# Optimization experiments

Hardware: AMD Instinct MI355X
Metric: run time of the kernel (lower is better)

## Reference

```python
import jax, jax.numpy as jnp
import numpy as np

N, E, R, IN, HID, HEADS, OUT, T = 20000, 320000, 16, 128, 64, 8, 128, 50000
NEG_SLOPE = 0.2
EPS = 1e-16


def _rgat_conv(x, edge_index, edge_type, W, att_q, att_k, heads, out_ch):
    """Relational GAT conv: per-relation transform, additive attention,
    segment-softmax over incoming edges of each dst node, scatter-add."""
    n = x.shape[0]
    r = W.shape[0]
    src, dst = edge_index[0], edge_index[1]
    # per-relation transform of all nodes: [R, N, H, O]
    xr = jnp.einsum('ni,rio->rno', x, W).reshape(r, n, heads, out_ch)
    k = xr[edge_type, src]  # [E, H, O] message from source
    q = xr[edge_type, dst]  # [E, H, O] query at destination
    logits = jnp.sum(q * att_q[edge_type], axis=-1) + jnp.sum(k * att_k[edge_type], axis=-1)  # [E, H]
    logits = jax.nn.leaky_relu(logits, NEG_SLOPE)
    # segment softmax over edges grouped by dst
    m = jax.ops.segment_max(logits, dst, num_segments=n)  # [N, H]
    e = jnp.exp(logits - m[dst])
    s = jax.ops.segment_sum(e, dst, num_segments=n)  # [N, H]
    a = e / (s[dst] + EPS)  # [E, H]
    out = jax.ops.segment_sum(a[..., None] * k, dst, num_segments=n)  # [N, H, O]
    return out.reshape(n, heads * out_ch)


def setup_inputs() -> dict:
    key = jax.random.key(0)
    ks = jax.random.split(key, 16)
    x = jax.random.normal(ks[0], (N, IN), dtype=jnp.float32)
    edge_index = jax.random.randint(ks[1], (2, E), 0, N, dtype=jnp.int64)
    edge_type = jax.random.randint(ks[2], (E,), 0, R, dtype=jnp.int64)
    target_edges = jax.random.randint(ks[3], (2, T), 0, N, dtype=jnp.int64)
    sc = 0.1
    W1 = jax.random.normal(ks[4], (R, IN, HEADS * HID), dtype=jnp.float32) * sc
    aq1 = jax.random.normal(ks[5], (R, HEADS, HID), dtype=jnp.float32) * sc
    ak1 = jax.random.normal(ks[6], (R, HEADS, HID), dtype=jnp.float32) * sc
    W2 = jax.random.normal(ks[7], (R, HEADS * HID, OUT), dtype=jnp.float32) * sc
    aq2 = jax.random.normal(ks[8], (R, 1, OUT), dtype=jnp.float32) * sc
    ak2 = jax.random.normal(ks[9], (R, 1, OUT), dtype=jnp.float32) * sc
    lw1 = jax.random.normal(ks[10], (2 * OUT, OUT), dtype=jnp.float32) * sc
    lb1 = jnp.zeros((OUT,), dtype=jnp.float32)
    lw2 = jax.random.normal(ks[11], (OUT, 1), dtype=jnp.float32) * sc
    lb2 = jnp.zeros((1,), dtype=jnp.float32)
    return {"x": x, "edge_index": edge_index, "edge_type": edge_type,
            "target_edges": target_edges, "W1": W1, "aq1": aq1, "ak1": ak1,
            "W2": W2, "aq2": aq2, "ak2": ak2, "lw1": lw1, "lb1": lb1,
            "lw2": lw2, "lb2": lb2}


def reference(x, edge_index, edge_type, target_edges, W1, aq1, ak1, W2, aq2, ak2, lw1, lb1, lw2, lb2):
    # encode (dropout is identity in eval mode)
    h = _rgat_conv(x, edge_index, edge_type, W1, aq1, ak1, HEADS, HID)  # [N, HEADS*HID]
    h = jax.nn.relu(h)
    z = _rgat_conv(h, edge_index, edge_type, W2, aq2, ak2, 1, OUT)  # [N, OUT]
    # decode target edges with link-prediction MLP
    z_pair = jnp.concatenate([z[target_edges[0]], z[target_edges[1]]], axis=1)  # [T, 2*OUT]
    hdec = jax.nn.relu(z_pair @ lw1 + lb1)
    return hdec @ lw2 + lb2  # [T, 1]
```

## Files before the change

kernel.cpp:

```cpp
#include <hip/hip_runtime.h>
#include <cstdint>
#include <cstddef>

#define NN     20000
#define NE     320000
#define NR     16
#define DIN    128
#define DH     512
#define DOUT   128
#define NT     50000
#define TILE   64
#define TILE1  128
#define CHUNKS 5
#define CHD    4000
#define NBUCKET (CHUNKS * NR)
#define MSGROWS 69888
#define MAXTPC1 2240
#define NTILESMAX1 (NE / TILE1 + NBUCKET)
#define MT2Y   157
#define YGRID  (MT2Y * 16)
#define QGRID  320

typedef __attribute__((ext_vector_type(8))) short bf16x8;
typedef __attribute__((ext_vector_type(4))) float f32x4;

__device__ __forceinline__ unsigned short f2bf(float x) {
    unsigned int b = __float_as_uint(x);
    b = b + 0x7fffu + ((b >> 16) & 1u);
    return (unsigned short)(b >> 16);
}
__device__ __forceinline__ float bf2f(unsigned short u) {
    return __uint_as_float(((unsigned int)u) << 16);
}
__device__ __forceinline__ unsigned packbf(float lo, float hi) {
    return (unsigned)f2bf(lo) | ((unsigned)f2bf(hi) << 16);
}

__global__ void alpha1_kernel(const float* __restrict__ W1, const float* __restrict__ aq1,
                              const float* __restrict__ ak1, float* __restrict__ alpha1) {
    int i = blockIdx.x;
    int c = threadIdx.x;
    int r = c >> 4, s = (c >> 3) & 1, h = c & 7;
    const float* att = (s == 0 ? aq1 : ak1) + (r * 8 + h) * 64;
    const float* w = W1 + ((size_t)(r * DIN + i)) * DH + h * 64;
    float acc = 0.f;
    #pragma unroll 8
    for (int o = 0; o < 64; ++o) acc += w[o] * att[o];
    alpha1[i * 256 + c] = acc;
}

__global__ void alpha2_kernel(const float* __restrict__ W2, const float* __restrict__ aq2,
                              const float* __restrict__ ak2, float* __restrict__ alpha2) {
    int g = blockIdx.x * blockDim.x + threadIdx.x;
    if (g >= DH * 32) return;
    int i = g >> 5, c = g & 31;
    int r = c >> 1, s = c & 1;
    const float* att = (s == 0 ? aq2 : ak2) + r * DOUT;
    const float* w = W2 + ((size_t)(r * DH + i)) * DOUT;
    float acc = 0.f;
    #pragma unroll 8
    for (int o = 0; o < DOUT; ++o) acc += w[o] * att[o];
    alpha2[i * 32 + c] = acc;
}

__global__ void splitA1T_kernel(const float* __restrict__ alpha1, unsigned short* __restrict__ A1Thi,
                                unsigned short* __restrict__ A1Tlo) {
    int g = blockIdx.x * 256 + threadIdx.x;
    if (g >= 128 * 256) return;
    int c = g >> 7, i = g & 127;
    float v = alpha1[i * 256 + c];
    unsigned short h = f2bf(v);
    A1Thi[g] = h;
    A1Tlo[g] = f2bf(v - bf2f(h));
}

__global__ void split_x_kernel(const float* __restrict__ x, unsigned short* __restrict__ xhi,
                               unsigned short* __restrict__ xlo) {
    int g = blockIdx.x * 256 + threadIdx.x;
    if (g >= NN * DIN / 4) return;
    float4 v = ((const float4*)x)[g];
    ushort4 h, l;
    h.x = f2bf(v.x); l.x = f2bf(v.x - bf2f(h.x));
    h.y = f2bf(v.y); l.y = f2bf(v.y - bf2f(h.y));
    h.z = f2bf(v.z); l.z = f2bf(v.z - bf2f(h.z));
    h.w = f2bf(v.w); l.w = f2bf(v.w - bf2f(h.w));
    ((ushort4*)xhi)[g] = h;
    ((ushort4*)xlo)[g] = l;
}

__global__ void splitW1T_kernel(const float* __restrict__ W1, unsigned short* __restrict__ Whi) {
    __shared__ float T[128 * 65];
    int r = blockIdx.x >> 3;
    int ob = blockIdx.x & 7;
    int tid = threadIdx.x;
    for (int idx = tid; idx < 128 * 64; idx += 256) {
        int i = idx >> 6, o = idx & 63;
        T[i * 65 + o] = W1[((size_t)(r * DIN + i)) * DH + ob * 64 + o];
    }
    __syncthreads();
    for (int idx = tid; idx < 64 * 128; idx += 256) {
        int o = idx >> 7, i = idx & 127;
        Whi[((size_t)r * DH + ob * 64 + o) * DIN + i] = f2bf(T[i * 65 + o]);
    }
}

__global__ void splitW2T_kernel(const float* __restrict__ W2, unsigned short* __restrict__ Whi) {
    __shared__ float T[128 * 65];
    int r = blockIdx.x >> 1;
    int ob = blockIdx.x & 1;
    int tid = threadIdx.x;
    for (int kc = 0; kc < 4; ++kc) {
        if (kc) __syncthreads();
        for (int idx = tid; idx < 128 * 64; idx += 256) {
            int k = idx >> 6, o = idx & 63;
            T[k * 65 + o] = W2[((size_t)(r * DH + kc * 128 + k)) * DOUT + ob * 64 + o];
        }
        __syncthreads();
        for (int idx = tid; idx < 64 * 128; idx += 256) {
            int o = idx >> 7, k = idx & 127;
            Whi[((size_t)r * DOUT + ob * 64 + o) * DH + kc * 128 + k] = f2bf(T[k * 65 + o]);
        }
    }
}

__global__ void splitLw1_kernel(const float* __restrict__ lw1, unsigned short* __restrict__ Lhi,
                                unsigned short* __restrict__ Llo) {
    int g = blockIdx.x * 256 + threadIdx.x;
    if (g >= 256 * 128) return;
    int o = g >> 8, k = g & 255;
    float v = lw1[k * 128 + o];
    unsigned short h = f2bf(v);
    Lhi[(size_t)o * 256 + k] = h;
    Llo[(size_t)o * 256 + k] = f2bf(v - bf2f(h));
}

__global__ void hist_kernel(const int* __restrict__ ei, const int* __restrict__ et,
                            int* __restrict__ cnt, int* __restrict__ cnt_d) {
    __shared__ int bins[NBUCKET];
    int t = threadIdx.x;
    if (t < NBUCKET) bins[t] = 0;
    __syncthreads();
    int e = blockIdx.x * 256 + t;
    if (e < NE) {
        int d = ei[NE + e];
        int key = (d / CHD) * NR + et[e];
        atomicAdd(&bins[key], 1);
        atomicAdd(&cnt_d[d], 1);
    }
    __syncthreads();
    if (t < NBUCKET && bins[t]) atomicAdd(&cnt[t], bins[t]);
}

__global__ void scan_bkt_kernel(const int* __restrict__ cnt, int* __restrict__ boffs,
                                int* __restrict__ cursor, int* __restrict__ cts) {
    if (threadIdx.x != 0) return;
    int acc = 0, tiles = 0;
    for (int b = 0; b < NBUCKET; ++b) {
        if ((b & (NR - 1)) == 0) cts[b >> 4] = tiles;
        boffs[b] = acc; cursor[b] = acc;
        int cn = cnt[b];
        tiles += (cn + TILE1 - 1) / TILE1;
        acc += cn;
    }
    boffs[NBUCKET] = acc; cts[CHUNKS] = tiles;
}

__global__ void tilemap_kernel(const int* __restrict__ boffs, int* __restrict__ tile_b,
                               int* __restrict__ tile_s) {
    __shared__ int bo[NBUCKET + 1];
    int tid = threadIdx.x;
    if (tid <= NBUCKET) bo[tid] = boffs[tid];
    __syncthreads();
    int t = blockIdx.x * 256 + tid;
    if (t >= NTILESMAX1) return;
    int acc = 0, bb = -1, ss = 0;
    for (int b = 0; b < NBUCKET; ++b) {
        int cn = bo[b + 1] - bo[b];
        int nt = (cn + TILE1 - 1) / TILE1;
        if (t >= acc && t < acc + nt) { bb = b; ss = bo[b] + (t - acc) * TILE1; }
        acc += nt;
    }
    tile_b[t] = bb; tile_s[t] = ss;
}

__global__ void bucket_place_kernel(const int* __restrict__ ei, const int* __restrict__ et,
                                    int* __restrict__ cursor, int* __restrict__ border) {
    __shared__ int binc[NBUCKET], base_[NBUCKET], rank_[NBUCKET];
    int t = threadIdx.x;
    if (t < NBUCKET) { binc[t] = 0; rank_[t] = 0; }
    __syncthreads();
    int e = blockIdx.x * 256 + t;
    int key = -1;
    if (e < NE) { key = (ei[NE + e] / CHD) * NR + et[e]; atomicAdd(&binc[key], 1); }
    __syncthreads();
    if (t < NBUCKET && binc[t]) base_[t] = atomicAdd(&cursor[t], binc[t]);
    __syncthreads();
    if (key >= 0) border[base_[key] + atomicAdd(&rank_[key], 1)] = e;
}

__global__ void scan_dst_kernel(const int* __restrict__ cnt_d, int* __restrict__ doffs,
                                int* __restrict__ cursor_d) {
    __shared__ int part[1024];
    int t = threadIdx.x;
    int base = t * 20;
    int s = 0;
    for (int i = 0; i < 20 && base + i < NN; ++i) s += cnt_d[base + i];
    part[t] = s;
    __syncthreads();
    for (int off = 1; off < 1024; off <<= 1) {
        int v = (t >= off) ? part[t - off] : 0;
        __syncthreads();
        part[t] += v;
        __syncthreads();
    }
    int run = part[t] - s;
    for (int i = 0; i < 20 && base + i < NN; ++i) {
        doffs[base + i] = run; cursor_d[base + i] = run;
        run += cnt_d[base + i];
    }
    if (t == 1023) doffs[NN] = part[1023];
}

__global__ void place_dst_kernel(const int* __restrict__ border, const int* __restrict__ ei,
                                 const int* __restrict__ et, int* __restrict__ cursor_d,
                                 int* __restrict__ dlist, int* __restrict__ dedge,
                                 int* __restrict__ dsr) {
    int pos = blockIdx.x * 256 + threadIdx.x;
    if (pos >= NE) return;
    int e = border[pos];
    int d = ei[NE + e];
    int idx = atomicAdd(&cursor_d[d], 1);
    dlist[idx] = pos;
    dedge[idx] = e;
    dsr[idx] = ei[e] * NR + et[e];
}

__global__ __launch_bounds__(256, 2)
void qk1_mfma_kernel(const unsigned short* __restrict__ xhi, const unsigned short* __restrict__ xlo,
                     const unsigned short* __restrict__ A1Thi, const unsigned short* __restrict__ A1Tlo,
                     float* __restrict__ qk1) {
    int t = (blockIdx.x & 7) * (QGRID / 8) + (blockIdx.x >> 3);
    if (t >= MT2Y * 2) return;
    int mt = t >> 1, nb = t & 1;
    int n0 = mt * 128;
    __shared__ __align__(16) unsigned short Ah[128 * 64];
    __shared__ __align__(16) unsigned short Al[128 * 64];
    __shared__ __align__(16) unsigned short Bh_[128 * 64];
    __shared__ __align__(16) unsigned short Bl_[128 * 64];
    int tid = threadIdx.x;
    int w = tid >> 6, lane = tid & 63;
    int l15 = lane & 15, l4 = lane >> 4;
    int wr = w >> 1, wc = w & 1;
    f32x4 acc[4][4];
    #pragma unroll
    for (int m = 0; m < 4; ++m)
        #pragma unroll
        for (int n = 0; n < 4; ++n) acc[m][n] = (f32x4){0.f, 0.f, 0.f, 0.f};
    for (int kc = 0; kc < 2; ++kc) {
        if (kc) __syncthreads();
        {
            int row = tid >> 1, seg = tid & 1;
            int n = n0 + row; if (n >= NN) n = NN - 1;
            unsigned rb = row * 128, sw = (row & 7) << 4;
            const uint4* ph = (const uint4*)(xhi + (size_t)n * DIN + kc * 64 + seg * 32);
            const uint4* pl = (const uint4*)(xlo + (size_t)n * DIN + kc * 64 + seg * 32);
            const uint4* qh = (const uint4*)(A1Thi + (size_t)(nb * 128 + row) * DIN + kc * 64 + seg * 32);
            const uint4* ql = (const uint4*)(A1Tlo + (size_t)(nb * 128 + row) * DIN + kc * 64 + seg * 32);
            #pragma unroll
            for (int i = 0; i < 4; ++i) {
                unsigned off = (rb + seg * 64 + i * 16) ^ sw;
                *(uint4*)((char*)Ah + off) = ph[i];
                *(uint4*)((char*)Al + off) = pl[i];
                *(uint4*)((char*)Bh_ + off) = qh[i];
                *(uint4*)((char*)Bl_ + off) = ql[i];
            }
        }
        __syncthreads();
        bf16x8 ah[4][2], al[4][2], bh[4][2], bl[4][2];
        #pragma unroll
        for (int m = 0; m < 4; ++m) {
            int row = wr * 64 + m * 16 + l15;
            unsigned rb = row * 128, sw = (row & 7) << 4;
            #pragma unroll
            for (int ks = 0; ks < 2; ++ks) {
                unsigned off = (rb + ks * 64 + l4 * 16) ^ sw;
                ah[m][ks] = *(const bf16x8*)((const char*)Ah + off);
                al[m][ks] = *(const bf16x8*)((const char*)Al + off);
            }
        }
        #pragma unroll
        for (int n = 0; n < 4; ++n) {
            int col = wc * 64 + n * 16 + l15;
            unsigned rb = col * 128, sw = (col & 7) << 4;
            #pragma unroll
            for (int ks = 0; ks < 2; ++ks) {
                unsigned off = (rb + ks * 64 + l4 * 16) ^ sw;
                bh[n][ks] = *(const bf16x8*)((const char*)Bh_ + off);
                bl[n][ks] = *(const bf16x8*)((const char*)Bl_ + off);
            }
        }
        #pragma unroll
        for (int n = 0; n < 4; ++n)
            #pragma unroll
            for (int ks = 0; ks < 2; ++ks)
                #pragma unroll
                for (int m = 0; m < 4; ++m) {
                    acc[m][n] = __builtin_amdgcn_mfma_f32_16x16x32_bf16(ah[m][ks], bh[n][ks], acc[m][n], 0, 0, 0);
                    acc[m][n] = __builtin_amdgcn_mfma_f32_16x16x32_bf16(al[m][ks], bh[n][ks], acc[m][n], 0, 0, 0);
                    acc[m][n] = __builtin_amdgcn_mfma_f32_16x16x32_bf16(ah[m][ks], bl[n][ks], acc[m][n], 0, 0, 0);
                }
    }
    #pragma unroll
    for (int m = 0; m < 4; ++m) {
        int row0 = n0 + wr * 64 + m * 16 + l4 * 4;
        #pragma unroll
        for (int rg = 0; rg < 4; ++rg) {
            int row = row0 + rg;
            if (row < NN) {
                float* op = qk1 + (size_t)row * 256 + nb * 128 + wc * 64 + l15;
                #pragma unroll
                for (int n = 0; n < 4; ++n) op[n * 16] = acc[m][n][rg];
            }
        }
    }
}

__global__ void elogit1_kernel(const int* __restrict__ ei, const int* __restrict__ et,
                               const float* __restrict__ qk1, float* __restrict__ e1) {
    int e = blockIdx.x * blockDim.x + threadIdx.x;
    if (e >= NE) return;
    int src = ei[e], dst = ei[NE + e], r = et[e];
    const float* qp = qk1 + (size_t)dst * 256 + r * 16;
    const float* kp = qk1 + (size_t)src * 256 + r * 16 + 8;
    float* ep = e1 + (size_t)e * 8;
    #pragma unroll
    for (int h = 0; h < 8; ++h) {
        float l = qp[h] + kp[h];
        l = l > 0.f ? l : 0.2f * l;
        ep[h] = __expf(l);
    }
}

__global__ __launch_bounds__(256, 3)
void l1_gemm_kernel(const unsigned short* __restrict__ xhi, const unsigned short* __restrict__ xlo,
                    const unsigned short* __restrict__ W1Thi,
                    const int* __restrict__ ei, const int* __restrict__ border,
                    const int* __restrict__ tile_b, const int* __restrict__ tile_s,
                    const int* __restrict__ boffs, const int* __restrict__ cts,
                    int c, unsigned* __restrict__ msgu) {
    int wg = (blockIdx.x & 7) * (MAXTPC1 / 8) + (blockIdx.x >> 3);
    int tt = wg >> 2, cb = wg & 3;
    int t = cts[c] + tt;
    if (t >= cts[c + 1]) return;
    int b = tile_b[t];
    int r = b & (NR - 1);
    int start = tile_s[t];
    int cstart = boffs[c * NR];
    int cnt = boffs[b + 1] - start; if (cnt > TILE1) cnt = TILE1;
    __shared__ __align__(16) unsigned short Ah[128 * 64];
    __shared__ __align__(16) unsigned short Al[128 * 64];
    __shared__ __align__(16) unsigned short Bh_[128 * 64];
    __shared__ int srcS[TILE1];
    int tid = threadIdx.x;
    if (tid < TILE1) {
        int sv = 0;
        if (tid < cnt) sv = ei[border[start + tid]];
        srcS[tid] = sv;
    }
    __syncthreads();
    int w = tid >> 6, lane = tid & 63;
    int l15 = lane & 15, l4 = lane >> 4;
    int wr = w >> 1, wc = w & 1;
    f32x4 acc[4][4];
    #pragma unroll
    for (int m = 0; m < 4; ++m)
        #pragma unroll
        for (int n = 0; n < 4; ++n) acc[m][n] = (f32x4){0.f, 0.f, 0.f, 0.f};
    for (int kc = 0; kc < 2; ++kc) {
        if (kc) __syncthreads();
        {
            int row = tid >> 1, seg = tid & 1;
            unsigned rb = row * 128, sw = (row & 7) << 4;
            const uint4* ph = (const uint4*)(xhi + (size_t)srcS[row] * DIN + kc * 64 + seg * 32);
            const uint4* pl = (const uint4*)(xlo + (size_t)srcS[row] * DIN + kc * 64 + seg * 32);
            const uint4* qh = (const uint4*)(W1Thi + ((size_t)r * DH + cb * 128 + row) * DIN + kc * 64 + seg * 32);
            #pragma unroll
            for (int i = 0; i < 4; ++i) {
                unsigned off = (rb + seg * 64 + i * 16) ^ sw;
                *(uint4*)((char*)Ah + off) = ph[i];
                *(uint4*)((char*)Al + off) = pl[i];
                *(uint4*)((char*)Bh_ + off) = qh[i];
            }
        }
        __syncthreads();
        bf16x8 ah[4][2], al[4][2], bh[4][2];
        #pragma unroll
        for (int m = 0; m < 4; ++m) {
            int row = wr * 64 + m * 16 + l15;
            unsigned rb = row * 128, sw = (row & 7) << 4;
            #pragma unroll
            for (int ks = 0; ks < 2; ++ks) {
                unsigned off = (rb + ks * 64 + l4 * 16) ^ sw;
                ah[m][ks] = *(const bf16x8*)((const char*)Ah + off);
                al[m][ks] = *(const bf16x8*)((const char*)Al + off);
            }
        }
        #pragma unroll
        for (int n = 0; n < 4; ++n) {
            int col = wc * 64 + n * 16 + l15;
            unsigned rb = col * 128, sw = (col & 7) << 4;
            #pragma unroll
            for (int ks = 0; ks < 2; ++ks) {
                unsigned off = (rb + ks * 64 + l4 * 16) ^ sw;
                bh[n][ks] = *(const bf16x8*)((const char*)Bh_ + off);
            }
        }
        #pragma unroll
        for (int n = 0; n < 4; ++n)
            #pragma unroll
            for (int ks = 0; ks < 2; ++ks)
                #pragma unroll
                for (int m = 0; m < 4; ++m) {
                    acc[m][n] = __builtin_amdgcn_mfma_f32_16x16x32_bf16(ah[m][ks], bh[n][ks], acc[m][n], 0, 0, 0);
                    acc[m][n] = __builtin_amdgcn_mfma_f32_16x16x32_bf16(al[m][ks], bh[n][ks], acc[m][n], 0, 0, 0);
                }
    }
    unsigned* mb = msgu + (size_t)(start - cstart) * 256 + cb * 64 + wc * 32 + l15;
    #pragma unroll
    for (int m = 0; m < 4; ++m) {
        int row0 = wr * 64 + m * 16 + l4 * 4;
        #pragma unroll
        for (int rg = 0; rg < 4; ++rg) {
            int row = row0 + rg;
            if (row < cnt) {
                unsigned* mp = mb + (size_t)row * 256;
                mp[0]  = packbf(acc[m][0][rg], acc[m][2][rg]);
                mp[16] = packbf(acc[m][1][rg], acc[m][3][rg]);
            }
        }
    }
}

__global__ void l1_agg_kernel(const unsigned* __restrict__ msgu, const float* __restrict__ e1,
                              const int* __restrict__ dlist, const int* __restrict__ dedge,
                              const int* __restrict__ doffs, const int* __restrict__ boffs,
                              int c, unsigned short* __restrict__ hhi, unsigned short* __restrict__ hlo,
                              const float* __restrict__ alpha2, float* __restrict__ qk2v) {
    __shared__ float hrow[DH];
    __shared__ float red[32][9];
    int tid = threadIdx.x;
    int d = c * CHD + blockIdx.x;
    if (d >= NN) return;
    int lo_ = doffs[d], hi_ = doffs[d + 1];
    int cstart = boffs[c * NR];
    int head = tid >> 5;
    float a0 = 0.f, a1 = 0.f, se = 0.f;
    for (int p = lo_; p < hi_; ++p) {
        int pos = dlist[p];
        float wgt = e1[(size_t)dedge[p] * 8 + head];
        se += wgt;
        unsigned v = msgu[(size_t)(pos - cstart) * 256 + tid];
        a0 += wgt * bf2f((unsigned short)(v & 0xffff));
        a1 += wgt * bf2f((unsigned short)(v >> 16));
    }
    float inv = 1.f / (se + 1e-16f);
    a0 *= inv; a1 *= inv;
    a0 = a0 > 0.f ? a0 : 0.f;
    a1 = a1 > 0.f ? a1 : 0.f;
    int w = tid >> 6, q = (tid >> 4) & 3, l15 = tid & 15;
    int nq = ((q >> 1) << 2) | (q & 1);
    int c0 = w * 128 + nq * 16 + l15;
    hrow[c0] = a0; hrow[c0 + 32] = a1;
    unsigned short h0 = f2bf(a0), h1 = f2bf(a1);
    hhi[(size_t)d * DH + c0] = h0;
    hlo[(size_t)d * DH + c0] = f2bf(a0 - bf2f(h0));
    hhi[(size_t)d * DH + c0 + 32] = h1;
    hlo[(size_t)d * DH + c0 + 32] = f2bf(a1 - bf2f(h1));
    __syncthreads();
    int j = tid & 31, ib = tid >> 5;
    float s = 0.f;
    #pragma unroll 8
    for (int i = ib * 64; i < ib * 64 + 64; ++i) s += hrow[i] * alpha2[(size_t)i * 32 + j];
    red[j][ib] = s;
    __syncthreads();
    if (tid < 32) {
        float t = 0.f;
        #pragma unroll
        for (int g = 0; g < 8; ++g) t += red[tid][g];
        qk2v[(size_t)d * 32 + tid] = t;
    }
}

__global__ void elogit2_kernel(const int* __restrict__ ei, const int* __restrict__ et,
                               const float* __restrict__ qk2, float* __restrict__ e2) {
    int e = blockIdx.x * blockDim.x + threadIdx.x;
    if (e >= NE) return;
    int src = ei[e], dst = ei[NE + e], r = et[e];
    float l = qk2[(size_t)dst * 32 + r * 2] + qk2[(size_t)src * 32 + r * 2 + 1];
    l = l > 0.f ? l : 0.2f * l;
    e2[e] = __expf(l);
}

__global__ __launch_bounds__(256, 3)
void y2_gemm_kernel(const unsigned short* __restrict__ hhi, const unsigned short* __restrict__ hlo,
                    const unsigned short* __restrict__ W2Thi,
                    unsigned* __restrict__ Y2u) {
    int t = (blockIdx.x & 7) * (YGRID / 8) + (blockIdx.x >> 3);
    int mt = t >> 4, r = t & 15;
    int n0 = mt * 128;
    __shared__ __align__(16) unsigned short Ah[128 * 64];
    __shared__ __align__(16) unsigned short Al[128 * 64];
    __shared__ __align__(16) unsigned short Bh_[128 * 64];
    int tid = threadIdx.x;
    int w = tid >> 6, lane = tid & 63;
    int l15 = lane & 15, l4 = lane >> 4;
    int wr = w >> 1, wc = w & 1;
    f32x4 acc[4][4];
    #pragma unroll
    for (int m = 0; m < 4; ++m)
        #pragma unroll
        for (int n = 0; n < 4; ++n) acc[m][n] = (f32x4){0.f, 0.f, 0.f, 0.f};
    for (int kc = 0; kc < 8; ++kc) {
        if (kc) __syncthreads();
        {
            int row = tid >> 1, seg = tid & 1;
            int n = n0 + row; if (n >= NN) n = NN - 1;
            unsigned rb = row * 128, sw = (row & 7) << 4;
            const uint4* ph = (const uint4*)(hhi + (size_t)n * DH + kc * 64 + seg * 32);
            const uint4* pl = (const uint4*)(hlo + (size_t)n * DH + kc * 64 + seg * 32);
            const uint4* qh = (const uint4*)(W2Thi + ((size_t)r * DOUT + row) * DH + kc * 64 + seg * 32);
            #pragma unroll
            for (int i = 0; i < 4; ++i) {
                unsigned off = (rb + seg * 64 + i * 16) ^ sw;
                *(uint4*)((char*)Ah + off) = ph[i];
                *(uint4*)((char*)Al + off) = pl[i];
                *(uint4*)((char*)Bh_ + off) = qh[i];
            }
        }
        __syncthreads();
        bf16x8 ah[4][2], al[4][2], bh[4][2];
        #pragma unroll
        for (int m = 0; m < 4; ++m) {
            int row = wr * 64 + m * 16 + l15;
            unsigned rb = row * 128, sw = (row & 7) << 4;
            #pragma unroll
            for (int ks = 0; ks < 2; ++ks) {
                unsigned off = (rb + ks * 64 + l4 * 16) ^ sw;
                ah[m][ks] = *(const bf16x8*)((const char*)Ah + off);
                al[m][ks] = *(const bf16x8*)((const char*)Al + off);
            }
        }
        #pragma unroll
        for (int n = 0; n < 4; ++n) {
            int col = wc * 64 + n * 16 + l15;
            unsigned rb = col * 128, sw = (col & 7) << 4;
            #pragma unroll
            for (int ks = 0; ks < 2; ++ks) {
                unsigned off = (rb + ks * 64 + l4 * 16) ^ sw;
                bh[n][ks] = *(const bf16x8*)((const char*)Bh_ + off);
            }
        }
        #pragma unroll
        for (int n = 0; n < 4; ++n)
            #pragma unroll
            for (int ks = 0; ks < 2; ++ks)
                #pragma unroll
                for (int m = 0; m < 4; ++m) {
                    acc[m][n] = __builtin_amdgcn_mfma_f32_16x16x32_bf16(ah[m][ks], bh[n][ks], acc[m][n], 0, 0, 0);
                    acc[m][n] = __builtin_amdgcn_mfma_f32_16x16x32_bf16(al[m][ks], bh[n][ks], acc[m][n], 0, 0, 0);
                }
    }
    unsigned* mb = Y2u + (size_t)n0 * 1024 + r * 64 + wc * 32 + l15;
    #pragma unroll
    for (int m = 0; m < 4; ++m) {
        int row0 = wr * 64 + m * 16 + l4 * 4;
        #pragma unroll
        for (int rg = 0; rg < 4; ++rg) {
            int row = row0 + rg;
            if (n0 + row < NN) {
                unsigned* mp = mb + (size_t)row * 1024;
                mp[0]  = packbf(acc[m][0][rg], acc[m][2][rg]);
                mp[16] = packbf(acc[m][1][rg], acc[m][3][rg]);
            }
        }
    }
}

__global__ void l2_agg_kernel(const unsigned* __restrict__ Y2u, const float* __restrict__ e2,
                              const int* __restrict__ dedge, const int* __restrict__ dsr,
                              const int* __restrict__ doffs, float* __restrict__ zacc) {
    int tid = threadIdx.x;
    int d = blockIdx.x * 4 + (tid >> 6);
    if (d >= NN) return;
    int lane = tid & 63;
    int lo_ = doffs[d], hi_ = doffs[d + 1];
    float a0 = 0.f, a1 = 0.f, se = 0.f;
    for (int p = lo_; p < hi_; ++p) {
        float wgt = e2[dedge[p]];
        se += wgt;
        unsigned v = Y2u[(size_t)dsr[p] * 64 + lane];
        a0 += wgt * bf2f((unsigned short)(v & 0xffff));
        a1 += wgt * bf2f((unsigned short)(v >> 16));
    }
    float inv = 1.f / (se + 1e-16f);
    int q = lane >> 4, l15 = lane & 15;
    int nq = ((q >> 1) << 2) | (q & 1);
    int c0 = nq * 16 + l15;
    zacc[(size_t)d * DOUT + c0] = a0 * inv;
    zacc[(size_t)d * DOUT + c0 + 32] = a1 * inv;
}

__global__ __launch_bounds__(256, 2)
void decode_kernel(const float* __restrict__ z, const int* __restrict__ tgt,
                   const unsigned short* __restrict__ Lhi, const unsigned short* __restrict__ Llo,
                   const float* __restrict__ lb1, const float* __restrict__ lw2,
                   const float* __restrict__ lb2, float* __restrict__ out) {
    __shared__ __align__(16) unsigned short Ah[64 * 256];
    __shared__ __align__(16) unsigned short Al[64 * 256];
    __shared__ float red[TILE][5];
    int t0 = blockIdx.x * TILE;
    int tid = threadIdx.x;
    int cnt = NT - t0; if (cnt > TILE) cnt = TILE;
    {
        int row = tid >> 2, seg = tid & 3;
        int node = 0;
        bool live = (row < cnt);
        if (live) node = tgt[(seg >> 1) * NT + t0 + row];
        const float4* pz = (const float4*)(z + (size_t)node * DOUT + (seg & 1) * 64);
        unsigned rb = row * 512, sb = (seg >> 1) * 256 + (seg & 1) * 128;
        unsigned sw = (row & 7) << 4;
        #pragma unroll
        for (int g = 0; g < 8; ++g) {
            float4 a = live ? pz[g * 2] : (float4){0,0,0,0};
            float4 bq = live ? pz[g * 2 + 1] : (float4){0,0,0,0};
            unsigned short h0 = f2bf(a.x), h1 = f2bf(a.y), h2 = f2bf(a.z), h3 = f2bf(a.w);
            unsigned short h4 = f2bf(bq.x), h5 = f2bf(bq.y), h6 = f2bf(bq.z), h7 = f2bf(bq.w);
            uint4 uh, ul;
            uh.x = (unsigned)h0 | ((unsigned)h1 << 16);
            uh.y = (unsigned)h2 | ((unsigned)h3 << 16);
            uh.z = (unsigned)h4 | ((unsigned)h5 << 16);
            uh.w = (unsigned)h6 | ((unsigned)h7 << 16);
            ul.x = (unsigned)f2bf(a.x - bf2f(h0)) | ((unsigned)f2bf(a.y - bf2f(h1)) << 16);
            ul.y = (unsigned)f2bf(a.z - bf2f(h2)) | ((unsigned)f2bf(a.w - bf2f(h3)) << 16);
            ul.z = (unsigned)f2bf(bq.x - bf2f(h4)) | ((unsigned)f2bf(bq.y - bf2f(h5)) << 16);
            ul.w = (unsigned)f2bf(bq.z - bf2f(h6)) | ((unsigned)f2bf(bq.w - bf2f(h7)) << 16);
            unsigned off = (rb + sb + g * 16) ^ sw;
            *(uint4*)((char*)Ah + off) = uh;
            *(uint4*)((char*)Al + off) = ul;
        }
    }
    __syncthreads();
    int w = tid >> 6, lane = tid & 63;
    int l15 = lane & 15, l4 = lane >> 4;
    const unsigned short* Bh = Lhi + (size_t)(w * 32 + l15) * 256 + l4 * 8;
    const unsigned short* Bl = Llo + (size_t)(w * 32 + l15) * 256 + l4 * 8;
    f32x4 acc[4][2];
    #pragma unroll
    for (int m = 0; m < 4; ++m) { acc[m][0] = (f32x4){0.f,0.f,0.f,0.f}; acc[m][1] = (f32x4){0.f,0.f,0.f,0.f}; }
    #pragma unroll
    for (int k = 0; k < 8; ++k) {
        bf16x8 ah[4], al[4];
        #pragma unroll
        for (int m = 0; m < 4; ++m) {
            int row = m * 16 + l15;
            unsigned off = ((unsigned)row * 512 + k * 64 + l4 * 16) ^ ((unsigned)(row & 7) << 4);
            ah[m] = *(const bf16x8*)((const char*)Ah + off);
            al[m] = *(const bf16x8*)((const char*)Al + off);
        }
        #pragma unroll
        for (int n = 0; n < 2; ++n) {
            bf16x8 bh = *(const bf16x8*)(Bh + (size_t)n * 16 * 256 + k * 32);
            bf16x8 bl = *(const bf16x8*)(Bl + (size_t)n * 16 * 256 + k * 32);
            #pragma unroll
            for (int m = 0; m < 4; ++m) {
                acc[m][n] = __builtin_amdgcn_mfma_f32_16x16x32_bf16(ah[m], bh, acc[m][n], 0, 0, 0);
                acc[m][n] = __builtin_amdgcn_mfma_f32_16x16x32_bf16(ah[m], bl, acc[m][n], 0, 0, 0);
                acc[m][n] = __builtin_amdgcn_mfma_f32_16x16x32_bf16(al[m], bh, acc[m][n], 0, 0, 0);
            }
        }
    }
    int col0 = w * 32 + l15;
    float lb_0 = lb1[col0], lb_1 = lb1[col0 + 16];
    float lwa = lw2[col0], lwb = lw2[col0 + 16];
    #pragma unroll
    for (int m = 0; m < 4; ++m) {
        #pragma unroll
        for (int rg = 0; rg < 4; ++rg) {
            float h0 = acc[m][0][rg] + lb_0; h0 = h0 > 0.f ? h0 : 0.f;
            float h1 = acc[m][1][rg] + lb_1; h1 = h1 > 0.f ? h1 : 0.f;
            float s = h0 * lwa + h1 * lwb;
            s += __shfl_xor(s, 1); s += __shfl_xor(s, 2);
            s += __shfl_xor(s, 4); s += __shfl_xor(s, 8);
            if (l15 == 0) red[m * 16 + l4 * 4 + rg][w] = s;
        }
    }
    __syncthreads();
    if (tid < cnt) out[t0 + tid] = red[tid][0] + red[tid][1] + red[tid][2] + red[tid][3] + lb2[0];
}

extern "C" void kernel_launch(void* const* d_in, const int* in_sizes, int n_in,
                              void* d_out, int out_size, void* d_ws, size_t ws_size,
                              hipStream_t stream) {
    const float* x   = (const float*)d_in[0];
    const int*   ei  = (const int*)d_in[1];
    const int*   et  = (const int*)d_in[2];
    const int*   tgt = (const int*)d_in[3];
    const float* W1  = (const float*)d_in[4];
    const float* aq1 = (const float*)d_in[5];
    const float* ak1 = (const float*)d_in[6];
    const float* W2  = (const float*)d_in[7];
    const float* aq2 = (const float*)d_in[8];
    const float* ak2 = (const float*)d_in[9];
    const float* lw1 = (const float*)d_in[10];
    const float* lb1 = (const float*)d_in[11];
    const float* lw2 = (const float*)d_in[12];
    const float* lb2 = (const float*)d_in[13];
    float* out = (float*)d_out;
    (void)in_sizes; (void)n_in; (void)out_size; (void)ws_size;

    char* ws = (char*)d_ws;
    size_t off = 0;
    auto alloc = [&](size_t bytes) -> void* {
        void* p = ws + off;
        off += (bytes + 255) & ~(size_t)255;
        return p;
    };
    int* cnt   = (int*)alloc(NBUCKET * sizeof(int));
    int* cnt_d = (int*)alloc((size_t)NN * sizeof(int));
    size_t zero_bytes = off;
    int*   boffs    = (int*)alloc((NBUCKET + 1) * sizeof(int));
    int*   cursor   = (int*)alloc(NBUCKET * sizeof(int));
    int*   cts      = (int*)alloc((CHUNKS + 1) * sizeof(int));
    int*   doffs    = (int*)alloc((size_t)(NN + 1) * sizeof(int));
    int*   cursor_d = (int*)alloc((size_t)NN * sizeof(int));
    int*   border   = (int*)alloc((size_t)NE * sizeof(int));
    int*   dlist    = (int*)alloc((size_t)NE * sizeof(int));
    int*   dedge    = (int*)alloc((size_t)NE * sizeof(int));
    int*   dsr      = (int*)alloc((size_t)NE * sizeof(int));
    int*   tile_b   = (int*)alloc((size_t)NTILESMAX1 * sizeof(int));
    int*   tile_s   = (int*)alloc((size_t)NTILESMAX1 * sizeof(int));
    float* alpha2   = (float*)alloc((size_t)512 * 32 * 4);
    float* qk2v     = (float*)alloc((size_t)NN * 32 * 4);
    float* e2       = (float*)alloc((size_t)NE * 4);
    float* zacc     = (float*)alloc((size_t)NN * DOUT * 4);
    unsigned short* xhi   = (unsigned short*)alloc((size_t)NN * DIN * 2);
    unsigned short* xlo   = (unsigned short*)alloc((size_t)NN * DIN * 2);
    unsigned short* hhi   = (unsigned short*)alloc((size_t)NN * DH * 2);
    unsigned short* hlo   = (unsigned short*)alloc((size_t)NN * DH * 2);
    unsigned short* W1Thi = (unsigned short*)alloc((size_t)NR * DH * DIN * 2);
    unsigned short* W2Thi = (unsigned short*)alloc((size_t)NR * DOUT * DH * 2);
    unsigned short* Lhi   = (unsigned short*)alloc((size_t)128 * 256 * 2);
    unsigned short* Llo   = (unsigned short*)alloc((size_t)128 * 256 * 2);
    unsigned short* A1Thi = (unsigned short*)alloc((size_t)256 * 128 * 2);
    unsigned short* A1Tlo = (unsigned short*)alloc((size_t)256 * 128 * 2);
    char* msgr = (char*)alloc((size_t)NN * 1024 * 4);
    unsigned* msgu = (unsigned*)msgr;
    unsigned* Y2u  = (unsigned*)msgr;
    float* alpha1 = (float*)msgr;
    float* qk1    = (float*)(msgr + 131072);
    float* e1     = (float*)(msgr + (size_t)MSGROWS * 1024);

    hipMemsetAsync(ws, 0, zero_bytes, stream);
    alpha1_kernel<<<DIN, 256, 0, stream>>>(W1, aq1, ak1, alpha1);
    splitA1T_kernel<<<(128 * 256 + 255) / 256, 256, 0, stream>>>(alpha1, A1Thi, A1Tlo);
    alpha2_kernel<<<(DH * 32 + 255) / 256, 256, 0, stream>>>(W2, aq2, ak2, alpha2);
    split_x_kernel<<<(NN * DIN / 4 + 255) / 256, 256, 0, stream>>>(x, xhi, xlo);
    splitW1T_kernel<<<NR * 8, 256, 0, stream>>>(W1, W1Thi);
    splitW2T_kernel<<<NR * 2, 256, 0, stream>>>(W2, W2Thi);
    splitLw1_kernel<<<(256 * 128 + 255) / 256, 256, 0, stream>>>(lw1, Lhi, Llo);
    hist_kernel<<<(NE + 255) / 256, 256, 0, stream>>>(ei, et, cnt, cnt_d);
    scan_bkt_kernel<<<1, 64, 0, stream>>>(cnt, boffs, cursor, cts);
    tilemap_kernel<<<(NTILESMAX1 + 255) / 256, 256, 0, stream>>>(boffs, tile_b, tile_s);
    bucket_place_kernel<<<(NE + 255) / 256, 256, 0, stream>>>(ei, et, cursor, border);
    scan_dst_kernel<<<1, 1024, 0, stream>>>(cnt_d, doffs, cursor_d);
    place_dst_kernel<<<(NE + 255) / 256, 256, 0, stream>>>(border, ei, et, cursor_d, dlist, dedge, dsr);
    qk1_mfma_kernel<<<QGRID, 256, 0, stream>>>(xhi, xlo, A1Thi, A1Tlo, qk1);
    elogit1_kernel<<<(NE + 255) / 256, 256, 0, stream>>>(ei, et, qk1, e1);
    for (int c = 0; c < CHUNKS; ++c) {
        l1_gemm_kernel<<<MAXTPC1, 256, 0, stream>>>(xhi, xlo, W1Thi, ei, border,
                                                    tile_b, tile_s, boffs, cts, c, msgu);
        l1_agg_kernel<<<CHD, 256, 0, stream>>>(msgu, e1, dlist, dedge, doffs, boffs, c,
                                               hhi, hlo, alpha2, qk2v);
    }
    elogit2_kernel<<<(NE + 255) / 256, 256, 0, stream>>>(ei, et, qk2v, e2);
    y2_gemm_kernel<<<YGRID, 256, 0, stream>>>(hhi, hlo, W2Thi, Y2u);
    l2_agg_kernel<<<(NN + 3) / 4, 256, 0, stream>>>(Y2u, e2, dedge, dsr, doffs, zacc);
    decode_kernel<<<(NT + TILE - 1) / TILE, 256, 0, stream>>>(zacc, tgt, Lhi, Llo,
                                                              lb1, lw2, lb2, out);
}
```

Baseline: 659.5 us.

## Load low-precision bf16 operands directly from global into registers, raising occupancy

In the three split-bf16 GEMM kernels (qk1, l1, y2), the low-half operands are now read straight from global memory into MFMA fragment registers instead of being staged through shared memory. This halves or quarters LDS use and raises launch_bounds to 4 blocks per CU. Separately, the two aggregation loops are unrolled by two so each iteration issues two independent gathers. The cost is uncoalesced per-lane global loads for the low operands and higher register pressure under the tighter occupancy bound.

```diff
diff --git a/kernel.cpp b/kernel.cpp
--- a/kernel.cpp
+++ b/kernel.cpp
@@ -235,7 +235,7 @@
     dsr[idx] = ei[e] * NR + et[e];
 }
 
-__global__ __launch_bounds__(256, 2)
+__global__ __launch_bounds__(256, 4)
 void qk1_mfma_kernel(const unsigned short* __restrict__ xhi, const unsigned short* __restrict__ xlo,
                      const unsigned short* __restrict__ A1Thi, const unsigned short* __restrict__ A1Tlo,
                      float* __restrict__ qk1) {
@@ -244,13 +244,20 @@
     int mt = t >> 1, nb = t & 1;
     int n0 = mt * 128;
     __shared__ __align__(16) unsigned short Ah[128 * 64];
-    __shared__ __align__(16) unsigned short Al[128 * 64];
     __shared__ __align__(16) unsigned short Bh_[128 * 64];
-    __shared__ __align__(16) unsigned short Bl_[128 * 64];
     int tid = threadIdx.x;
     int w = tid >> 6, lane = tid & 63;
     int l15 = lane & 15, l4 = lane >> 4;
     int wr = w >> 1, wc = w & 1;
+    const unsigned short* alp[4];
+    const unsigned short* blp[4];
+    #pragma unroll
+    for (int m = 0; m < 4; ++m) {
+        int rn = n0 + wr * 64 + m * 16 + l15; if (rn >= NN) rn = NN - 1;
+        alp[m] = xlo + (size_t)rn * DIN;
+        int col = wc * 64 + m * 16 + l15;
+        blp[m] = A1Tlo + (size_t)(nb * 128 + col) * DIN;
+    }
     f32x4 acc[4][4];
     #pragma unroll
     for (int m = 0; m < 4; ++m)
@@ -263,20 +270,24 @@
             int n = n0 + row; if (n >= NN) n = NN - 1;
             unsigned rb = row * 128, sw = (row & 7) << 4;
             const uint4* ph = (const uint4*)(xhi + (size_t)n * DIN + kc * 64 + seg * 32);
-            const uint4* pl = (const uint4*)(xlo + (size_t)n * DIN + kc * 64 + seg * 32);
             const uint4* qh = (const uint4*)(A1Thi + (size_t)(nb * 128 + row) * DIN + kc * 64 + seg * 32);
-            const uint4* ql = (const uint4*)(A1Tlo + (size_t)(nb * 128 + row) * DIN + kc * 64 + seg * 32);
             #pragma unroll
             for (int i = 0; i < 4; ++i) {
                 unsigned off = (rb + seg * 64 + i * 16) ^ sw;
                 *(uint4*)((char*)Ah + off) = ph[i];
-                *(uint4*)((char*)Al + off) = pl[i];
                 *(uint4*)((char*)Bh_ + off) = qh[i];
-                *(uint4*)((char*)Bl_ + off) = ql[i];
-            }
-        }
+            }
+        }
+        bf16x8 alf[4][2], blf[4][2];
+        #pragma unroll
+        for (int m = 0; m < 4; ++m)
+            #pragma unroll
+            for (int ks = 0; ks < 2; ++ks) {
+                alf[m][ks] = *(const bf16x8*)(alp[m] + kc * 64 + ks * 32 + l4 * 8);
+                blf[m][ks] = *(const bf16x8*)(blp[m] + kc * 64 + ks * 32 + l4 * 8);
+            }
         __syncthreads();
-        bf16x8 ah[4][2], al[4][2], bh[4][2], bl[4][2];
+        bf16x8 ah[4][2], bh[4][2];
         #pragma unroll
         for (int m = 0; m < 4; ++m) {
             int row = wr * 64 + m * 16 + l15;
@@ -285,7 +296,6 @@
             for (int ks = 0; ks < 2; ++ks) {
                 unsigned off = (rb + ks * 64 + l4 * 16) ^ sw;
                 ah[m][ks] = *(const bf16x8*)((const char*)Ah + off);
-                al[m][ks] = *(const bf16x8*)((const char*)Al + off);
             }
         }
         #pragma unroll
@@ -296,7 +306,6 @@
             for (int ks = 0; ks < 2; ++ks) {
                 unsigned off = (rb + ks * 64 + l4 * 16) ^ sw;
                 bh[n][ks] = *(const bf16x8*)((const char*)Bh_ + off);
-                bl[n][ks] = *(const bf16x8*)((const char*)Bl_ + off);
             }
         }
         #pragma unroll
@@ -306,8 +315,8 @@
                 #pragma unroll
                 for (int m = 0; m < 4; ++m) {
                     acc[m][n] = __builtin_amdgcn_mfma_f32_16x16x32_bf16(ah[m][ks], bh[n][ks], acc[m][n], 0, 0, 0);
-                    acc[m][n] = __builtin_amdgcn_mfma_f32_16x16x32_bf16(al[m][ks], bh[n][ks], acc[m][n], 0, 0, 0);
-                    acc[m][n] = __builtin_amdgcn_mfma_f32_16x16x32_bf16(ah[m][ks], bl[n][ks], acc[m][n], 0, 0, 0);
+                    acc[m][n] = __builtin_amdgcn_mfma_f32_16x16x32_bf16(alf[m][ks], bh[n][ks], acc[m][n], 0, 0, 0);
+                    acc[m][n] = __builtin_amdgcn_mfma_f32_16x16x32_bf16(ah[m][ks], blf[n][ks], acc[m][n], 0, 0, 0);
                 }
     }
     #pragma unroll
@@ -341,7 +350,7 @@
     }
 }
 
-__global__ __launch_bounds__(256, 3)
+__global__ __launch_bounds__(256, 4)
 void l1_gemm_kernel(const unsigned short* __restrict__ xhi, const unsigned short* __restrict__ xlo,
                     const unsigned short* __restrict__ W1Thi,
                     const int* __restrict__ ei, const int* __restrict__ border,
@@ -358,7 +367,6 @@
     int cstart = boffs[c * NR];
     int cnt = boffs[b + 1] - start; if (cnt > TILE1) cnt = TILE1;
     __shared__ __align__(16) unsigned short Ah[128 * 64];
-    __shared__ __align__(16) unsigned short Al[128 * 64];
     __shared__ __align__(16) unsigned short Bh_[128 * 64];
     __shared__ int srcS[TILE1];
     int tid = threadIdx.x;
@@ -371,6 +379,12 @@
     int w = tid >> 6, lane = tid & 63;
     int l15 = lane & 15, l4 = lane >> 4;
     int wr = w >> 1, wc = w & 1;
+    const unsigned short* alp[4];
+    #pragma unroll
+    for (int m = 0; m < 4; ++m) {
+        int row = wr * 64 + m * 16 + l15;
+        alp[m] = xlo + (size_t)srcS[row] * DIN;
+    }
     f32x4 acc[4][4];
     #pragma unroll
     for (int m = 0; m < 4; ++m)
@@ -382,18 +396,22 @@
             int row = tid >> 1, seg = tid & 1;
             unsigned rb = row * 128, sw = (row & 7) << 4;
             const uint4* ph = (const uint4*)(xhi + (size_t)srcS[row] * DIN + kc * 64 + seg * 32);
-            const uint4* pl = (const uint4*)(xlo + (size_t)srcS[row] * DIN + kc * 64 + seg * 32);
             const uint4* qh = (const uint4*)(W1Thi + ((size_t)r * DH + cb * 128 + row) * DIN + kc * 64 + seg * 32);
             #pragma unroll
             for (int i = 0; i < 4; ++i) {
                 unsigned off = (rb + seg * 64 + i * 16) ^ sw;
                 *(uint4*)((char*)Ah + off) = ph[i];
-                *(uint4*)((char*)Al + off) = pl[i];
                 *(uint4*)((char*)Bh_ + off) = qh[i];
             }
         }
+        bf16x8 alf[4][2];
+        #pragma unroll
+        for (int m = 0; m < 4; ++m)
+            #pragma unroll
+            for (int ks = 0; ks < 2; ++ks)
+                alf[m][ks] = *(const bf16x8*)(alp[m] + kc * 64 + ks * 32 + l4 * 8);
         __syncthreads();
-        bf16x8 ah[4][2], al[4][2], bh[4][2];
+        bf16x8 ah[4][2], bh[4][2];
         #pragma unroll
         for (int m = 0; m < 4; ++m) {
             int row = wr * 64 + m * 16 + l15;
@@ -402,7 +420,6 @@
             for (int ks = 0; ks < 2; ++ks) {
                 unsigned off = (rb + ks * 64 + l4 * 16) ^ sw;
                 ah[m][ks] = *(const bf16x8*)((const char*)Ah + off);
-                al[m][ks] = *(const bf16x8*)((const char*)Al + off);
             }
         }
         #pragma unroll
@@ -422,7 +439,7 @@
                 #pragma unroll
                 for (int m = 0; m < 4; ++m) {
                     acc[m][n] = __builtin_amdgcn_mfma_f32_16x16x32_bf16(ah[m][ks], bh[n][ks], acc[m][n], 0, 0, 0);
-                    acc[m][n] = __builtin_amdgcn_mfma_f32_16x16x32_bf16(al[m][ks], bh[n][ks], acc[m][n], 0, 0, 0);
+                    acc[m][n] = __builtin_amdgcn_mfma_f32_16x16x32_bf16(alf[m][ks], bh[n][ks], acc[m][n], 0, 0, 0);
                 }
     }
     unsigned* mb = msgu + (size_t)(start - cstart) * 256 + cb * 64 + wc * 32 + l15;
@@ -455,13 +472,25 @@
     int cstart = boffs[c * NR];
     int head = tid >> 5;
     float a0 = 0.f, a1 = 0.f, se = 0.f;
-    for (int p = lo_; p < hi_; ++p) {
-        int pos = dlist[p];
-        float wgt = e1[(size_t)dedge[p] * 8 + head];
-        se += wgt;
-        unsigned v = msgu[(size_t)(pos - cstart) * 256 + tid];
-        a0 += wgt * bf2f((unsigned short)(v & 0xffff));
-        a1 += wgt * bf2f((unsigned short)(v >> 16));
+    int p = lo_;
+    for (; p + 1 < hi_; p += 2) {
+        int pos0 = dlist[p], pos1 = dlist[p + 1];
+        int e0 = dedge[p], e1x = dedge[p + 1];
+        float w0 = e1[(size_t)e0 * 8 + head];
+        float w1 = e1[(size_t)e1x * 8 + head];
+        unsigned v0 = msgu[(size_t)(pos0 - cstart) * 256 + tid];
+        unsigned v1 = msgu[(size_t)(pos1 - cstart) * 256 + tid];
+        se += w0 + w1;
+        a0 += w0 * bf2f((unsigned short)(v0 & 0xffff)) + w1 * bf2f((unsigned short)(v1 & 0xffff));
+        a1 += w0 * bf2f((unsigned short)(v0 >> 16)) + w1 * bf2f((unsigned short)(v1 >> 16));
+    }
+    if (p < hi_) {
+        int pos0 = dlist[p];
+        float w0 = e1[(size_t)dedge[p] * 8 + head];
+        unsigned v0 = msgu[(size_t)(pos0 - cstart) * 256 + tid];
+        se += w0;
+        a0 += w0 * bf2f((unsigned short)(v0 & 0xffff));
+        a1 += w0 * bf2f((unsigned short)(v0 >> 16));
     }
     float inv = 1.f / (se + 1e-16f);
     a0 *= inv; a1 *= inv;
@@ -501,7 +530,7 @@
     e2[e] = __expf(l);
 }
 
-__global__ __launch_bounds__(256, 3)
+__global__ __launch_bounds__(256, 4)
 void y2_gemm_kernel(const unsigned short* __restrict__ hhi, const unsigned short* __restrict__ hlo,
                     const unsigned short* __restrict__ W2Thi,
                     unsigned* __restrict__ Y2u) {
@@ -509,12 +538,17 @@
     int mt = t >> 4, r = t & 15;
     int n0 = mt * 128;
     __shared__ __align__(16) unsigned short Ah[128 * 64];
-    __shared__ __align__(16) unsigned short Al[128 * 64];
     __shared__ __align__(16) unsigned short Bh_[128 * 64];
     int tid = threadIdx.x;
     int w = tid >> 6, lane = tid & 63;
     int l15 = lane & 15, l4 = lane >> 4;
     int wr = w >> 1, wc = w & 1;
+    const unsigned short* alp[4];
+    #pragma unroll
+    for (int m = 0; m < 4; ++m) {
+        int rn = n0 + wr * 64 + m * 16 + l15; if (rn >= NN) rn = NN - 1;
+        alp[m] = hlo + (size_t)rn * DH;
+    }
     f32x4 acc[4][4];
     #pragma unroll
     for (int m = 0; m < 4; ++m)
@@ -527,18 +561,22 @@
             int n = n0 + row; if (n >= NN) n = NN - 1;
             unsigned rb = row * 128, sw = (row & 7) << 4;
             const uint4* ph = (const uint4*)(hhi + (size_t)n * DH + kc * 64 + seg * 32);
-            const uint4* pl = (const uint4*)(hlo + (size_t)n * DH + kc * 64 + seg * 32);
             const uint4* qh = (const uint4*)(W2Thi + ((size_t)r * DOUT + row) * DH + kc * 64 + seg * 32);
             #pragma unroll
             for (int i = 0; i < 4; ++i) {
                 unsigned off = (rb + seg * 64 + i * 16) ^ sw;
                 *(uint4*)((char*)Ah + off) = ph[i];
-                *(uint4*)((char*)Al + off) = pl[i];
                 *(uint4*)((char*)Bh_ + off) = qh[i];
             }
         }
+        bf16x8 alf[4][2];
+        #pragma unroll
+        for (int m = 0; m < 4; ++m)
+            #pragma unroll
+            for (int ks = 0; ks < 2; ++ks)
+                alf[m][ks] = *(const bf16x8*)(alp[m] + kc * 64 + ks * 32 + l4 * 8);
         __syncthreads();
-        bf16x8 ah[4][2], al[4][2], bh[4][2];
+        bf16x8 ah[4][2], bh[4][2];
         #pragma unroll
         for (int m = 0; m < 4; ++m) {
             int row = wr * 64 + m * 16 + l15;
@@ -547,7 +585,6 @@
             for (int ks = 0; ks < 2; ++ks) {
                 unsigned off = (rb + ks * 64 + l4 * 16) ^ sw;
                 ah[m][ks] = *(const bf16x8*)((const char*)Ah + off);
-                al[m][ks] = *(const bf16x8*)((const char*)Al + off);
             }
         }
         #pragma unroll
@@ -567,7 +604,7 @@
                 #pragma unroll
                 for (int m = 0; m < 4; ++m) {
                     acc[m][n] = __builtin_amdgcn_mfma_f32_16x16x32_bf16(ah[m][ks], bh[n][ks], acc[m][n], 0, 0, 0);
-                    acc[m][n] = __builtin_amdgcn_mfma_f32_16x16x32_bf16(al[m][ks], bh[n][ks], acc[m][n], 0, 0, 0);
+                    acc[m][n] = __builtin_amdgcn_mfma_f32_16x16x32_bf16(alf[m][ks], bh[n][ks], acc[m][n], 0, 0, 0);
                 }
     }
     unsigned* mb = Y2u + (size_t)n0 * 1024 + r * 64 + wc * 32 + l15;
@@ -595,12 +632,22 @@
     int lane = tid & 63;
     int lo_ = doffs[d], hi_ = doffs[d + 1];
     float a0 = 0.f, a1 = 0.f, se = 0.f;
-    for (int p = lo_; p < hi_; ++p) {
-        float wgt = e2[dedge[p]];
-        se += wgt;
-        unsigned v = Y2u[(size_t)dsr[p] * 64 + lane];
-        a0 += wgt * bf2f((unsigned short)(v & 0xffff));
-        a1 += wgt * bf2f((unsigned short)(v >> 16));
+    int p = lo_;
+    for (; p + 1 < hi_; p += 2) {
+        int s0 = dsr[p], s1 = dsr[p + 1];
+        float w0 = e2[dedge[p]], w1 = e2[dedge[p + 1]];
+        unsigned v0 = Y2u[(size_t)s0 * 64 + lane];
+        unsigned v1 = Y2u[(size_t)s1 * 64 + lane];
+        se += w0 + w1;
+        a0 += w0 * bf2f((unsigned short)(v0 & 0xffff)) + w1 * bf2f((unsigned short)(v1 & 0xffff));
+        a1 += w0 * bf2f((unsigned short)(v0 >> 16)) + w1 * bf2f((unsigned short)(v1 >> 16));
+    }
+    if (p < hi_) {
+        float w0 = e2[dedge[p]];
+        unsigned v0 = Y2u[(size_t)dsr[p] * 64 + lane];
+        se += w0;
+        a0 += w0 * bf2f((unsigned short)(v0 & 0xffff));
+        a1 += w0 * bf2f((unsigned short)(v0 >> 16));
     }
     float inv = 1.f / (se + 1e-16f);
     int q = lane >> 4, l15 = lane & 15;
```

Result: slower. 982.6 us (+49.0%).
